# Optimization experiments

Measured on AMD Instinct MI355X. Metric: run time of the kernel, lower is better.

The kernel has to match this reference:

```python
import jax, jax.numpy as jnp
import numpy as np


def _forward(x, wc, we, Wb1, bb1, Wb2, bb2, Wr1, br1, Wr2, br2,
             Wq1, bq1, Wq2, bq2, Wq3, bq3, Wo1, bo1, Wo2, bo2, Wo3, bo3, scale):
    bs, c, h, w = x.shape
    Hs, Ws = scale * h, scale * w
    fh = (jnp.arange(Hs, dtype=jnp.float32) + 0.5) / scale
    fw = (jnp.arange(Ws, dtype=jnp.float32) + 0.5) / scale
    coor_h = fh - jnp.floor(fh + 0.001) - 0.5  # [Hs] fractional phase
    coor_w = fw - jnp.floor(fw + 0.001) - 0.5  # [Ws]
    ones_hw = jnp.ones((Hs, Ws), jnp.float32)
    meta = jnp.stack([ones_hw, ones_hw / scale,
                      jnp.broadcast_to(coor_h[:, None], (Hs, Ws)),
                      jnp.broadcast_to(coor_w[None, :], (Hs, Ws))], 0)  # [4,Hs,Ws]
    chan_mean = x.mean(axis=(0, 2, 3))  # [c]
    chan_scale = jnp.concatenate([chan_mean[:, None], jnp.ones((c, 3), jnp.float32)], axis=1)  # [c,4]
    inp = meta[None] * chan_scale[:, :, None, None]  # [c,4,Hs,Ws]

    # body: 1x1x1 Conv3d over spectral-channel axis c
    lin = lambda W, b, t: jnp.einsum('oc,cfhw->ofhw', W, t) + b[:, None, None, None]
    emb = jax.nn.relu(lin(Wb2, bb2, jax.nn.relu(lin(Wb1, bb1, inp))))  # [c,4,Hs,Ws]

    # offset head: Conv2d 1x1 with batch = c, features = 4 -> 2
    lin2 = lambda W, b, t: jnp.einsum('of,cfhw->cohw', W, t) + b[None, :, None, None]
    off = lin2(Wo3, bo3, jax.nn.relu(lin2(Wo2, bo2, jax.nn.relu(lin2(Wo1, bo1, emb)))))  # [c,2,Hs,Ws]

    # routing_1: Conv3d over c -> 1 channel, sigmoid
    r = jax.nn.sigmoid(lin(Wr2, br2, jax.nn.relu(lin(Wr1, br1, emb))))[0]  # [4,Hs,Ws]
    # routing_2: Conv2d 1x1 over the 4 meta-features -> E experts
    lin3 = lambda W, b, t: jnp.einsum('of,fhw->ohw', W, t) + b[:, None, None]
    rw = jax.nn.sigmoid(lin3(Wq3, bq3, jax.nn.relu(lin3(Wq2, bq2, jax.nn.relu(lin3(Wq1, bq1, r))))))  # [E,Hs,Ws]

    # per-channel offset grid_sample (bilinear, zeros padding, align_corners=True)
    px0 = fw - 0.5  # [Ws] base source x coord
    py0 = fh - 0.5  # [Hs]

    def sample(img, offx, offy):  # img [bs,h,w]; off* [Hs,Ws]
        px = px0[None, :] + offx
        py = py0[:, None] + offy
        x0 = jnp.floor(px); y0 = jnp.floor(py)
        wx = px - x0; wy = py - y0
        x0i = x0.astype(jnp.int32); y0i = y0.astype(jnp.int32)
        def g(yi, xi):
            v = ((xi >= 0) & (xi <= w - 1) & (yi >= 0) & (yi <= h - 1)).astype(img.dtype)
            return img[:, jnp.clip(yi, 0, h - 1), jnp.clip(xi, 0, w - 1)] * v[None]
        return (g(y0i, x0i) * ((1 - wy) * (1 - wx))[None]
                + g(y0i, x0i + 1) * ((1 - wy) * wx)[None]
                + g(y0i + 1, x0i) * (wy * (1 - wx))[None]
                + g(y0i + 1, x0i + 1) * (wy * wx)[None])

    fea0 = jax.vmap(lambda xi, oi: sample(xi, oi[0], oi[1]),
                    in_axes=(1, 0), out_axes=1)(x, off)  # [bs,c,Hs,Ws]

    # per-pixel expert-mixed compress/expand: (sum_e r_e Wc_e) f then (sum_e r_e We_e)
    mid = jnp.einsum('ehw,ekc,bchw->bkhw', rw, wc, fea0)   # [bs,c//8,Hs,Ws]
    out = jnp.einsum('ehw,eck,bkhw->bchw', rw, we, mid)    # [bs,c,Hs,Ws]
    return out + fea0


def setup_inputs() -> dict:
    key = jax.random.key(0)
    ks = jax.random.split(key, 32)
    bs, c, h, w = 4, 64, 64, 64
    E, k = 4, c // 8
    s = 0.05
    d = {
        'x': jax.random.normal(ks[0], (bs, c, h, w), jnp.float32),
        'wc': jax.random.normal(ks[1], (E, k, c), jnp.float32) * s,
        'we': jax.random.normal(ks[2], (E, c, k), jnp.float32) * s,
        'Wb1': jax.random.normal(ks[3], (c, c), jnp.float32) * s,
        'bb1': jax.random.normal(ks[4], (c,), jnp.float32) * s,
        'Wb2': jax.random.normal(ks[5], (c, c), jnp.float32) * s,
        'bb2': jax.random.normal(ks[6], (c,), jnp.float32) * s,
        'Wr1': jax.random.normal(ks[7], (64, c), jnp.float32) * s,
        'br1': jax.random.normal(ks[8], (64,), jnp.float32) * s,
        'Wr2': jax.random.normal(ks[9], (1, 64), jnp.float32) * s,
        'br2': jax.random.normal(ks[10], (1,), jnp.float32) * s,
        'Wq1': jax.random.normal(ks[11], (64, 4), jnp.float32) * s,
        'bq1': jax.random.normal(ks[12], (64,), jnp.float32) * s,
        'Wq2': jax.random.normal(ks[13], (64, 64), jnp.float32) * s,
        'bq2': jax.random.normal(ks[14], (64,), jnp.float32) * s,
        'Wq3': jax.random.normal(ks[15], (E, 64), jnp.float32) * s,
        'bq3': jax.random.normal(ks[16], (E,), jnp.float32) * s,
        'Wo1': jax.random.normal(ks[17], (64, 4), jnp.float32) * s,
        'bo1': jax.random.normal(ks[18], (64,), jnp.float32) * s,
        'Wo2': jax.random.normal(ks[19], (64, 64), jnp.float32) * s,
        'bo2': jax.random.normal(ks[20], (64,), jnp.float32) * s,
        'Wo3': jax.random.normal(ks[21], (2, 64), jnp.float32) * s,
        'bo3': jax.random.normal(ks[22], (2,), jnp.float32) * s,
        'scale': 4,
    }
    return d


def reference(x, wc, we, Wb1, bb1, Wb2, bb2, Wr1, br1, Wr2, br2,
              Wq1, bq1, Wq2, bq2, Wq3, bq3, Wo1, bo1, Wo2, bo2, Wo3, bo3, scale):
    return _forward(x, wc, we, Wb1, bb1, Wb2, bb2, Wr1, br1, Wr2, br2,
                    Wq1, bq1, Wq2, bq2, Wq3, bq3, Wo1, bo1, Wo2, bo2, Wo3, bo3, int(scale))
```

## Files before the change

### kernel.cpp

```cpp
#include <hip/hip_runtime.h>


__device__ __forceinline__ float relu_(float v){ return fmaxf(v, 0.f); }
__device__ __forceinline__ float sigm_(float v){ return 1.f/(1.f + __expf(-v)); }

__global__ void k_mean(const float* __restrict__ x, float* __restrict__ ws) {
  const int ch = blockIdx.x, b = blockIdx.y, t = threadIdx.x;
  const float* xp = x + (size_t)(b*64 + ch)*4096;
  const float4* p4 = reinterpret_cast<const float4*>(xp);
  float4 v0 = p4[t], v1 = p4[t+256], v2 = p4[t+512], v3 = p4[t+768];
  float s = ((v0.x+v0.y)+(v0.z+v0.w)) + ((v1.x+v1.y)+(v1.z+v1.w))
          + ((v2.x+v2.y)+(v2.z+v2.w)) + ((v3.x+v3.y)+(v3.z+v3.w));
  __shared__ float red[256];
  red[t] = s; __syncthreads();
  for (int off = 128; off > 0; off >>= 1) {
    if (t < off) red[t] += red[t + off];
    __syncthreads();
  }
  if (t == 0) ws[b*64 + ch] = red[0];

  float* dst = ws + 2113792 + (size_t)(b*64 + ch)*4752;
  if (t < 66) {
    float4* drow = reinterpret_cast<float4*>(dst + t*72);
    const float4 z = make_float4(0.f, 0.f, 0.f, 0.f);
    if (t == 0 || t == 65) {
      #pragma unroll
      for (int q = 0; q < 18; ++q) drow[q] = z;
    } else {
      const float4* srow = reinterpret_cast<const float4*>(xp + (t-1)*64);
      drow[0] = z;
      #pragma unroll
      for (int q = 0; q < 16; ++q) drow[1+q] = srow[q];
      drow[17] = z;
    }
  }
}

__launch_bounds__(256)
__global__ void k_phase(const float* __restrict__ wc, const float* __restrict__ we,
    const float* __restrict__ Wb1, const float* __restrict__ bb1,
    const float* __restrict__ Wb2, const float* __restrict__ bb2,
    const float* __restrict__ Wr1, const float* __restrict__ br1,
    const float* __restrict__ Wr2, const float* __restrict__ br2,
    const float* __restrict__ Wq1, const float* __restrict__ bq1,
    const float* __restrict__ Wq2, const float* __restrict__ bq2,
    const float* __restrict__ Wq3, const float* __restrict__ bq3,
    const float* __restrict__ Wo1, const float* __restrict__ bo1,
    const float* __restrict__ Wo2, const float* __restrict__ bo2,
    const float* __restrict__ Wo3, const float* __restrict__ bo3,
    float* __restrict__ ws)
{
  const int p = blockIdx.x, pi = p >> 2, pj = p & 3;
  const int t = threadIdx.x;
  const float chv = 0.25f*pi - 0.375f, cwv = 0.25f*pj - 0.375f;

  __shared__ float WbL1[64*66];
  __shared__ float WbL2[64*66];
  __shared__ float WrL1[64*66];
  __shared__ float WqL2[64*66];
  __shared__ __align__(16) float Wo2L[4096];
  __shared__ __align__(16) float Wo1L[256];
  __shared__ __align__(16) float wcL[2048];
  __shared__ __align__(16) float weL[2048];
  __shared__ float Wo3L[128];
  __shared__ float Wq1L[256], Wq3L[256];
  __shared__ float Wr2L[64];
  __shared__ float bb1L[64], bb2L[64], br1L[64], bq1L[64], bq2L[64];
  __shared__ float bo1L[64], bo2L[64];

  __shared__ float meanL[64];
  __shared__ __align__(16) float t1L[64][4];
  __shared__ __align__(16) float embL[64][4];
  __shared__ __align__(16) float rpL[64][4];
  __shared__ float r4[4];
  __shared__ float q1L[64], q2L[64];
  __shared__ float rwL[4];
  __shared__ float oxL[64][4], oyL[64][4];
  __shared__ float oxF[64], oyF[64];

  {
    const float* srcs[4] = {Wb1, Wb2, Wr1, Wq2};
    float* dsts[4] = {WbL1, WbL2, WrL1, WqL2};
    for (int m = 0; m < 4; ++m) {
      const float4* W4 = reinterpret_cast<const float4*>(srcs[m]);
      float* WL = dsts[m];
      for (int v = t; v < 1024; v += 256) {
        float4 d = W4[v];
        const int r = v >> 4, c = (v & 15) << 2;
        float* q = &WL[r*66 + c];
        q[0] = d.x; q[1] = d.y; q[2] = d.z; q[3] = d.w;
      }
    }
    for (int v = t; v < 1024; v += 256)
      reinterpret_cast<float4*>(Wo2L)[v] = reinterpret_cast<const float4*>(Wo2)[v];
    for (int v = t; v < 512; v += 256) {
      reinterpret_cast<float4*>(wcL)[v] = reinterpret_cast<const float4*>(wc)[v];
      reinterpret_cast<float4*>(weL)[v] = reinterpret_cast<const float4*>(we)[v];
    }
    if (t < 64) {
      reinterpret_cast<float4*>(Wo1L)[t] = reinterpret_cast<const float4*>(Wo1)[t];
      reinterpret_cast<float4*>(Wq1L)[t] = reinterpret_cast<const float4*>(Wq1)[t];
      reinterpret_cast<float4*>(Wq3L)[t] = reinterpret_cast<const float4*>(Wq3)[t];
      bb1L[t] = bb1[t]; bb2L[t] = bb2[t]; br1L[t] = br1[t];
      bq1L[t] = bq1[t]; bq2L[t] = bq2[t];
      bo1L[t] = bo1[t]; bo2L[t] = bo2[t];
      Wr2L[t] = Wr2[t];
      const float* wsp = ws;
      meanL[t] = (wsp[t] + wsp[64+t] + wsp[128+t] + wsp[192+t]) * (1.f/16384.f);
    }
    if (t >= 64 && t < 192) Wo3L[t-64] = Wo3[t-64];
  }
  __syncthreads();

  if (t < 64) {
    float a0 = 0.f, as = 0.f;
    const float* row = &WbL1[t*66];
    #pragma unroll 8
    for (int c = 0; c < 64; ++c) { float w = row[c]; a0 += w*meanL[c]; as += w; }
    float bb = bb1L[t];
    t1L[t][0] = relu_(a0 + bb);
    t1L[t][1] = relu_(0.25f*as + bb);
    t1L[t][2] = relu_(chv*as + bb);
    t1L[t][3] = relu_(cwv*as + bb);
  }
  __syncthreads();
  if (t < 64) {
    float bb = bb2L[t];
    float e0=bb,e1=bb,e2=bb,e3=bb;
    const float* row = &WbL2[t*66];
    #pragma unroll 8
    for (int c = 0; c < 64; ++c) {
      float w = row[c];
      float4 tv = *reinterpret_cast<const float4*>(&t1L[c][0]);
      e0 += w*tv.x; e1 += w*tv.y; e2 += w*tv.z; e3 += w*tv.w;
    }
    embL[t][0]=relu_(e0); embL[t][1]=relu_(e1); embL[t][2]=relu_(e2); embL[t][3]=relu_(e3);
  }
  __syncthreads();
  if (t < 64) {
    float bb = br1L[t];
    float p0=bb,p1=bb,p2=bb,p3=bb;
    const float* row = &WrL1[t*66];
    #pragma unroll 8
    for (int c = 0; c < 64; ++c) {
      float w = row[c];
      float4 ev = *reinterpret_cast<const float4*>(&embL[c][0]);
      p0 += w*ev.x; p1 += w*ev.y; p2 += w*ev.z; p3 += w*ev.w;
    }
    rpL[t][0]=relu_(p0); rpL[t][1]=relu_(p1); rpL[t][2]=relu_(p2); rpL[t][3]=relu_(p3);
  }
  __syncthreads();
  if (t < 4) {
    float acc = br2[0];
    #pragma unroll 8
    for (int c = 0; c < 64; ++c) acc += Wr2L[c]*rpL[c][t];
    r4[t] = sigm_(acc);
  }
  __syncthreads();
  if (t < 64) {
    float acc = bq1L[t];
    #pragma unroll
    for (int f = 0; f < 4; ++f) acc += Wq1L[t*4+f]*r4[f];
    q1L[t] = relu_(acc);
  }
  __syncthreads();
  if (t < 64) {
    float acc = bq2L[t];
    const float* row = &WqL2[t*66];
    #pragma unroll 8
    for (int c = 0; c < 64; ++c) acc += row[c]*q1L[c];
    q2L[t] = relu_(acc);
  }
  __syncthreads();
  if (t < 4) {
    float acc = bq3[t];
    #pragma unroll 8
    for (int c = 0; c < 64; ++c) acc += Wq3L[t*64+c]*q2L[c];
    rwL[t] = sigm_(acc);
  }
  __syncthreads();

  {
    const int ch = t & 63, q = t >> 6;
    const float4 e = *reinterpret_cast<const float4*>(&embL[ch][0]);
    float v1[64];
    #pragma unroll
    for (int o = 0; o < 64; ++o) {
      float4 w = *reinterpret_cast<const float4*>(&Wo1L[o*4]);
      v1[o] = relu_(w.x*e.x + w.y*e.y + w.z*e.z + w.w*e.w + bo1L[o]);
    }
    float ox = 0.f, oy = 0.f;
    for (int o = q*16; o < q*16+16; ++o) {
      float acc = bo2L[o];
      const float4* row = reinterpret_cast<const float4*>(&Wo2L[o*64]);
      #pragma unroll
      for (int k = 0; k < 16; ++k) {
        float4 w = row[k];
        acc += w.x*v1[4*k+0] + w.y*v1[4*k+1] + w.z*v1[4*k+2] + w.w*v1[4*k+3];
      }
      acc = relu_(acc);
      ox += Wo3L[o]*acc;
      oy += Wo3L[64+o]*acc;
    }
    oxL[ch][q] = ox; oyL[ch][q] = oy;
  }
  __syncthreads();
  if (t < 64) {
    oxF[t] = oxL[t][0]+oxL[t][1]+oxL[t][2]+oxL[t][3] + bo3[0];
    oyF[t] = oyL[t][0]+oyL[t][1]+oyL[t][2]+oyL[t][3] + bo3[1];
  }
  __syncthreads();

  {
    const float r0 = rwL[0], r1 = rwL[1], r2 = rwL[2], r3 = rwL[3];
    for (int idx = t; idx < 1024; idx += 256) {
      const int ch = idx >> 4, k = idx & 15;
      float v;
      if (k < 8) {
        v = r0*wcL[(0*8+k)*64+ch] + r1*wcL[(1*8+k)*64+ch]
          + r2*wcL[(2*8+k)*64+ch] + r3*wcL[(3*8+k)*64+ch];
      } else {
        const int kk = k - 8;
        v = r0*weL[(0*64+ch)*8+kk] + r1*weL[(1*64+ch)*8+kk]
          + r2*weL[(2*64+ch)*8+kk] + r3*weL[(3*64+ch)*8+kk];
      }
      ws[256 + (p*64+ch)*16 + k] = v;
    }
  }

  {
    const int ch = t & 63, iq = t >> 6;
    const float oy = oyF[ch];
    const float B = 0.25f*pj - 0.375f + oxF[ch];
    const float bxf = floorf(B);
    const float wx = B - bxf;
    const float wx0 = 1.f - wx, wx1 = wx;
    const int bx = min(max((int)bxf, -4), 3);
    const int chbase = ch*4752 + 4 + bx;
    float4* dst = reinterpret_cast<float4*>(ws + 16640 + (size_t)p*131072);
    for (int n = 0; n < 64; ++n) {
      const int i = iq*64 + n;
      const float py = i*0.25f - 0.375f + oy;
      const float fy = floorf(py);
      const float wy = py - fy;
      const int y0 = (int)fy, y1 = y0 + 1;
      const int y0c = min(max(y0, -1), 64), y1c = min(max(y1, -1), 64);
      const float wy0 = ((unsigned)y0 <= 63u) ? (1.f - wy) : 0.f;
      const float wy1 = ((unsigned)y1 <= 63u) ? wy : 0.f;
      float4 A, Bq;
      A.x = __int_as_float(chbase + (y0c+1)*72);
      A.y = __int_as_float(chbase + (y1c+1)*72);
      A.z = wy0*wx0; A.w = wy0*wx1;
      Bq.x = wy1*wx0; Bq.y = wy1*wx1; Bq.z = 0.f; Bq.w = 0.f;
      dst[(i*64 + ch)*2 + 0] = A;
      dst[(i*64 + ch)*2 + 1] = Bq;
    }
  }
}

__launch_bounds__(256, 3)
__global__ void k_main(const float* __restrict__ ws, float* __restrict__ out) {
  const int i = blockIdx.x;
  const int b = blockIdx.y;
  const int w = __builtin_amdgcn_readfirstlane((int)(threadIdx.x >> 6));
  const int l = threadIdx.x & 63;
  const int p = (i & 3)*4 + w;

  const float* __restrict__ wmx = ws + 256 + p*1024;
  const float* __restrict__ yr  = ws + 16640 + (size_t)p*131072 + (size_t)i*512;
  const float* __restrict__ xpb = ws + 2113792 + (size_t)b*304128;

  __shared__ float tile[4096];

  float fea[64];
  float m0=0.f,m1=0.f,m2=0.f,m3=0.f,m4=0.f,m5=0.f,m6=0.f,m7=0.f;

  #pragma unroll
  for (int ch = 0; ch < 64; ++ch) {
    const float4 ra = *reinterpret_cast<const float4*>(yr + ch*8);
    const float4 rb = *reinterpret_cast<const float4*>(yr + ch*8 + 4);
    const float4 wa = *reinterpret_cast<const float4*>(wmx + ch*16);
    const float4 wb = *reinterpret_cast<const float4*>(wmx + ch*16 + 4);
    const int r0 = __float_as_int(ra.x), r1 = __float_as_int(ra.y);
    const float g00 = xpb[r0 + l], g01 = xpb[r0 + l + 1];
    const float g10 = xpb[r1 + l], g11 = xpb[r1 + l + 1];
    const float fv = g00*ra.z + g01*ra.w + g10*rb.x + g11*rb.y;
    fea[ch] = fv;
    m0 += wa.x*fv; m1 += wa.y*fv; m2 += wa.z*fv; m3 += wa.w*fv;
    m4 += wb.x*fv; m5 += wb.y*fv; m6 += wb.z*fv; m7 += wb.w*fv;
  }

  float* __restrict__ ob = out + (size_t)b*4194304 + i*256;
  const int sw = (w & 1) << 4;
  #pragma unroll
  for (int c4 = 0; c4 < 4; ++c4) {
    #pragma unroll
    for (int cc = 0; cc < 16; ++cc) {
      const int ch = c4*16 + cc;
      const float4 wa = *reinterpret_cast<const float4*>(wmx + ch*16 + 8);
      const float4 wb = *reinterpret_cast<const float4*>(wmx + ch*16 + 12);
      float acc = fea[ch];
      acc += wa.x*m0 + wa.y*m1 + wa.z*m2 + wa.w*m3;
      acc += wb.x*m4 + wb.y*m5 + wb.z*m6 + wb.w*m7;
      tile[cc*256 + w*64 + (l ^ sw)] = acc;
    }
    __syncthreads();
    #pragma unroll
    for (int cc = 0; cc < 16; ++cc) {
      const int ch = c4*16 + cc;
      const float v = tile[cc*256 + (l&3)*64 + ((w*16 + (l>>2)) ^ ((l&1)<<4))];
      ob[ch*65536 + w*64 + l] = v;
    }
    __syncthreads();
  }
}

extern "C" void kernel_launch(void* const* d_in, const int* in_sizes, int n_in,
                              void* d_out, int out_size, void* d_ws, size_t ws_size,
                              hipStream_t stream) {
  const float* x   = (const float*)d_in[0];
  const float* wc  = (const float*)d_in[1];
  const float* we  = (const float*)d_in[2];
  const float* Wb1 = (const float*)d_in[3];
  const float* bb1 = (const float*)d_in[4];
  const float* Wb2 = (const float*)d_in[5];
  const float* bb2 = (const float*)d_in[6];
  const float* Wr1 = (const float*)d_in[7];
  const float* br1 = (const float*)d_in[8];
  const float* Wr2 = (const float*)d_in[9];
  const float* br2 = (const float*)d_in[10];
  const float* Wq1 = (const float*)d_in[11];
  const float* bq1 = (const float*)d_in[12];
  const float* Wq2 = (const float*)d_in[13];
  const float* bq2 = (const float*)d_in[14];
  const float* Wq3 = (const float*)d_in[15];
  const float* bq3 = (const float*)d_in[16];
  const float* Wo1 = (const float*)d_in[17];
  const float* bo1 = (const float*)d_in[18];
  const float* Wo2 = (const float*)d_in[19];
  const float* bo2 = (const float*)d_in[20];
  const float* Wo3 = (const float*)d_in[21];
  const float* bo3 = (const float*)d_in[22];
  float* ws  = (float*)d_ws;
  float* out = (float*)d_out;

  k_mean<<<dim3(64, 4), 256, 0, stream>>>(x, ws);
  k_phase<<<16, 256, 0, stream>>>(wc, we, Wb1, bb1, Wb2, bb2, Wr1, br1, Wr2, br2,
                                  Wq1, bq1, Wq2, bq2, Wq3, bq3,
                                  Wo1, bo1, Wo2, bo2, Wo3, bo3, ws);
  k_main<<<dim3(256, 4), 256, 0, stream>>>(ws, out);
}
```

Before: 195.9 us.

## Compute per-row sampling coefficients in main kernel instead of precomputed table

```diff
diff --git a/kernel.cpp b/kernel.cpp
--- a/kernel.cpp
+++ b/kernel.cpp
@@ -19,7 +19,7 @@
   }
   if (t == 0) ws[b*64 + ch] = red[0];
 
-  float* dst = ws + 2113792 + (size_t)(b*64 + ch)*4752;
+  float* dst = ws + 20736 + (size_t)(b*64 + ch)*4752;
   if (t < 66) {
     float4* drow = reinterpret_cast<float4*>(dst + t*72);
     const float4 z = make_float4(0.f, 0.f, 0.f, 0.f);
@@ -228,63 +228,73 @@
     }
   }
 
-  {
-    const int ch = t & 63, iq = t >> 6;
-    const float oy = oyF[ch];
-    const float B = 0.25f*pj - 0.375f + oxF[ch];
+  if (t < 64) {
+    const float B = 0.25f*pj - 0.375f + oxF[t];
     const float bxf = floorf(B);
     const float wx = B - bxf;
-    const float wx0 = 1.f - wx, wx1 = wx;
     const int bx = min(max((int)bxf, -4), 3);
-    const int chbase = ch*4752 + 4 + bx;
-    float4* dst = reinterpret_cast<float4*>(ws + 16640 + (size_t)p*131072);
-    for (int n = 0; n < 64; ++n) {
-      const int i = iq*64 + n;
-      const float py = i*0.25f - 0.375f + oy;
-      const float fy = floorf(py);
-      const float wy = py - fy;
-      const int y0 = (int)fy, y1 = y0 + 1;
-      const int y0c = min(max(y0, -1), 64), y1c = min(max(y1, -1), 64);
-      const float wy0 = ((unsigned)y0 <= 63u) ? (1.f - wy) : 0.f;
-      const float wy1 = ((unsigned)y1 <= 63u) ? wy : 0.f;
-      float4 A, Bq;
-      A.x = __int_as_float(chbase + (y0c+1)*72);
-      A.y = __int_as_float(chbase + (y1c+1)*72);
-      A.z = wy0*wx0; A.w = wy0*wx1;
-      Bq.x = wy1*wx0; Bq.y = wy1*wx1; Bq.z = 0.f; Bq.w = 0.f;
-      dst[(i*64 + ch)*2 + 0] = A;
-      dst[(i*64 + ch)*2 + 1] = Bq;
-    }
+    float4 r;
+    r.x = __int_as_float(t*4752 + 4 + bx);
+    r.y = 1.f - wx;
+    r.z = wx;
+    r.w = oyF[t];
+    *reinterpret_cast<float4*>(ws + 16640 + (p*64 + t)*4) = r;
   }
 }
 
-__launch_bounds__(256, 3)
+__launch_bounds__(256, 4)
 __global__ void k_main(const float* __restrict__ ws, float* __restrict__ out) {
   const int i = blockIdx.x;
   const int b = blockIdx.y;
   const int w = __builtin_amdgcn_readfirstlane((int)(threadIdx.x >> 6));
   const int l = threadIdx.x & 63;
-  const int p = (i & 3)*4 + w;
-
-  const float* __restrict__ wmx = ws + 256 + p*1024;
-  const float* __restrict__ yr  = ws + 16640 + (size_t)p*131072 + (size_t)i*512;
-  const float* __restrict__ xpb = ws + 2113792 + (size_t)b*304128;
-
+  const int t = threadIdx.x;
+  const int pi4 = (i & 3)*4;
+
+  const float* __restrict__ xpb = ws + 20736 + (size_t)b*304128;
+
+  __shared__ __align__(16) float wmxL[4096];
+  __shared__ __align__(16) float pcfL[1024];
   __shared__ float tile[4096];
+
+  {
+    const float4* s1 = reinterpret_cast<const float4*>(ws + 256 + pi4*1024);
+    float4* d1 = reinterpret_cast<float4*>(wmxL);
+    d1[t] = s1[t];
+    d1[t+256] = s1[t+256];
+    d1[t+512] = s1[t+512];
+    d1[t+768] = s1[t+768];
+    const float4* s2 = reinterpret_cast<const float4*>(ws + 16640 + pi4*256);
+    reinterpret_cast<float4*>(pcfL)[t] = s2[t];
+  }
+  __syncthreads();
+
+  const float* __restrict__ wmxw = &wmxL[w*1024];
+  const float* __restrict__ pcfw = &pcfL[w*256];
+  const float fi = i*0.25f - 0.375f;
 
   float fea[64];
   float m0=0.f,m1=0.f,m2=0.f,m3=0.f,m4=0.f,m5=0.f,m6=0.f,m7=0.f;
 
   #pragma unroll
   for (int ch = 0; ch < 64; ++ch) {
-    const float4 ra = *reinterpret_cast<const float4*>(yr + ch*8);
-    const float4 rb = *reinterpret_cast<const float4*>(yr + ch*8 + 4);
-    const float4 wa = *reinterpret_cast<const float4*>(wmx + ch*16);
-    const float4 wb = *reinterpret_cast<const float4*>(wmx + ch*16 + 4);
-    const int r0 = __float_as_int(ra.x), r1 = __float_as_int(ra.y);
+    const float4 c = *reinterpret_cast<const float4*>(pcfw + ch*4);
+    const float4 wa = *reinterpret_cast<const float4*>(wmxw + ch*16);
+    const float4 wb = *reinterpret_cast<const float4*>(wmxw + ch*16 + 4);
+    const int base = __float_as_int(c.x);
+    const float wx0 = c.y, wx1 = c.z;
+    const float py = fi + c.w;
+    const float fy = floorf(py);
+    const float wy = py - fy;
+    const int y0 = (int)fy, y1 = y0 + 1;
+    const int y0c = min(max(y0, -1), 64), y1c = min(max(y1, -1), 64);
+    const float wy0 = ((unsigned)y0 <= 63u) ? (1.f - wy) : 0.f;
+    const float wy1 = ((unsigned)y1 <= 63u) ? wy : 0.f;
+    const int r0 = base + (y0c+1)*72, r1 = base + (y1c+1)*72;
+    const float a0 = wy0*wx0, a1 = wy0*wx1, a2 = wy1*wx0, a3 = wy1*wx1;
     const float g00 = xpb[r0 + l], g01 = xpb[r0 + l + 1];
     const float g10 = xpb[r1 + l], g11 = xpb[r1 + l + 1];
-    const float fv = g00*ra.z + g01*ra.w + g10*rb.x + g11*rb.y;
+    const float fv = g00*a0 + g01*a1 + g10*a2 + g11*a3;
     fea[ch] = fv;
     m0 += wa.x*fv; m1 += wa.y*fv; m2 += wa.z*fv; m3 += wa.w*fv;
     m4 += wb.x*fv; m5 += wb.y*fv; m6 += wb.z*fv; m7 += wb.w*fv;
@@ -297,8 +307,8 @@
     #pragma unroll
     for (int cc = 0; cc < 16; ++cc) {
       const int ch = c4*16 + cc;
-      const float4 wa = *reinterpret_cast<const float4*>(wmx + ch*16 + 8);
-      const float4 wb = *reinterpret_cast<const float4*>(wmx + ch*16 + 12);
+      const float4 wa = *reinterpret_cast<const float4*>(wmxw + ch*16 + 8);
+      const float4 wb = *reinterpret_cast<const float4*>(wmxw + ch*16 + 12);
       float acc = fea[ch];
       acc += wa.x*m0 + wa.y*m1 + wa.z*m2 + wa.w*m3;
       acc += wb.x*m4 + wb.y*m5 + wb.z*m6 + wb.w*m7;
```

Result: faster. 168.2 us (-14.2%).
